# Performance work log

Hardware: AMD Instinct MI355X
Metric: run time of the kernel (lower is better)

Reference implementation:

```python
import jax, jax.numpy as jnp
import numpy as np

# dims: B=batch, CIN/COUT=channels, T=timesteps, K=kernel length (= T+1, since
# max_timesteps=2048 is even and CKConv bumps it to odd), DK=SIREN hidden width
B, CIN, COUT, T, DK = 32, 32, 32, 2048, 32
K = T + 1


def setup_inputs() -> dict:
    key = jax.random.key(0)
    ks = jax.random.split(key, 9)
    u = lambda k, shape, lim: jax.random.uniform(k, shape, minval=-lim, maxval=lim)
    # SIREN layer 1 (Conv1d 1->DK, k=1): first layer init uniform(-1, 1)
    w1 = u(ks[0], (DK, 1), 1.0)
    b1 = u(ks[1], (DK,), 1.0)          # torch bias init: U(-1/sqrt(fan_in)), fan_in=1
    # SIREN layer 2 (DK->DK): uniform(-sqrt(6/DK)/omega0, +), omega0=1
    siren_val = float(np.sqrt(6.0 / DK))
    w2 = u(ks[2], (DK, DK), siren_val)
    b2 = u(ks[3], (DK,), float(1.0 / np.sqrt(DK)))
    # output layer (DK -> CIN*COUT)
    w3 = u(ks[4], (CIN * COUT, DK), siren_val)
    b3 = u(ks[5], (CIN * COUT,), float(1.0 / np.sqrt(DK)))
    omega1 = jnp.asarray(1.0, jnp.float32)
    omega2 = jnp.asarray(1.0, jnp.float32)
    bias = jax.random.normal(ks[6], (COUT,), jnp.float32)   # CKConv output bias
    x = jax.random.normal(ks[7], (B, CIN, T), jnp.float32)
    rel_pos = jnp.linspace(-1.0, 1.0, K, dtype=jnp.float32)  # buffer _rel_positions
    return dict(x=x, rel_pos=rel_pos, w1=w1, b1=b1, omega1=omega1,
                w2=w2, b2=b2, omega2=omega2, w3=w3, b3=b3, bias=bias)


def reference(x, rel_pos, w1, b1, omega1, w2, b2, omega2, w3, b3, bias):
    # --- SIREN kernel network: 1x1 convs over the K positions == matmuls ---
    pos = rel_pos[None, :]                                   # (1, K)
    h = jnp.sin(omega1 * (w1 @ pos + b1[:, None]))           # (DK, K)
    h = jnp.sin(omega2 * (w2 @ h + b2[:, None]))             # (DK, K)
    kern = (w3 @ h + b3[:, None]).reshape(COUT, CIN, K)      # (COUT, CIN, K)
    # --- causal conv: left-pad by K-1 zeros, then valid cross-correlation ---
    out = jax.lax.conv_general_dilated(
        x, kern, window_strides=(1,), padding=[(K - 1, 0)],
        dimension_numbers=("NCH", "OIH", "NCH"))             # (B, COUT, T)
    return out + bias[None, :, None]
```

## Files before the change

### kernel.cpp

```cpp
#include <hip/hip_runtime.h>
#include <hip/hip_bf16.h>
#include <stdint.h>

typedef short bf16x8 __attribute__((ext_vector_type(8)));
typedef float f32x16 __attribute__((ext_vector_type(16)));

#define T 2048
#define KLEN 2049
#define DK 32
#define NCO 32
#define NCI 32
#define NB 32

#define GR 2216
#define SREF 2055
#define WT_CH 257
#define WT_ELEMS (NCI*WT_CH*NCO*8)
#define XR_ELEMS (NB*NCI*GR)

#define WT_OFF 0
#define XR_OFF (WT_ELEMS*2)
#define XRS_OFF (XR_OFF + XR_ELEMS*2)

#define CIB 528
#define GPC 1056
#define GPCP 1088
#define CPYB 17472
#define BUFB (2*CPYB)
#define LDS_TOT (2*BUFB)

__global__ __launch_bounds__(256) void gen_w(
    const float* __restrict__ rel_pos,
    const float* __restrict__ w1, const float* __restrict__ b1, const float* __restrict__ om1,
    const float* __restrict__ w2, const float* __restrict__ b2, const float* __restrict__ om2,
    const float* __restrict__ w3, const float* __restrict__ b3,
    uint16_t* __restrict__ Wt)
{
    __shared__ float h1s[8][32];
    __shared__ float h2s[8][32];
    int t = threadIdx.x;
    int dchunk = blockIdx.x;
    int dd = t >> 5, i = t & 31;
    int d = (dchunk << 3) + dd;
    float pos = (d < KLEN) ? rel_pos[2048 - d] : 0.f;
    h1s[dd][i] = sinf(om1[0] * (w1[i] * pos + b1[i]));
    __syncthreads();
    {
        float a = b2[i];
        #pragma unroll
        for (int j = 0; j < 32; ++j) a += w2[i*32 + j] * h1s[dd][j];
        h2s[dd][i] = sinf(om2[0] * a);
    }
    __syncthreads();
    for (int r = 0; r < 4; ++r) {
        int tt = t + (r << 8);
        int ci = tt >> 5, co = tt & 31;
        int coci = (co << 5) + ci;
        float w3r[32];
        #pragma unroll
        for (int j = 0; j < 8; ++j)
            *(float4*)&w3r[j*4] = *(const float4*)&w3[coci*32 + j*4];
        float bb = b3[coci];
        union { uint16_t u[8]; uint4 q; } pack;
        #pragma unroll
        for (int ddd = 0; ddd < 8; ++ddd) {
            float a = bb;
            #pragma unroll
            for (int j = 0; j < 32; ++j) a += w3r[j] * h2s[ddd][j];
            if (((dchunk << 3) + ddd) >= KLEN) a = 0.f;
            __hip_bfloat16 hv = __float2bfloat16(a);
            pack.u[ddd] = *(uint16_t*)&hv;
        }
        *(uint4*)&Wt[((ci*WT_CH + dchunk)*NCO + co) << 3] = pack.q;
    }
}

__global__ __launch_bounds__(256) void gen_x(const float* __restrict__ x,
                                             uint16_t* __restrict__ xr,
                                             uint16_t* __restrict__ xrs)
{
    int idx = blockIdx.x*256 + threadIdx.x;
    if (idx >= NB*NCI*GR) return;
    int row = idx / GR;
    int g = idx - row*GR;
    int s = SREF - g;
    float v  = (s  >= 0 && s  < T) ? x[row*T + s]  : 0.f;
    int s2 = s - 1;
    float v2 = (s2 >= 0 && s2 < T) ? x[row*T + s2] : 0.f;
    __hip_bfloat16 hv = __float2bfloat16(v);
    __hip_bfloat16 hv2 = __float2bfloat16(v2);
    xr[idx]  = *(uint16_t*)&hv;
    xrs[idx] = *(uint16_t*)&hv2;
}

__device__ __forceinline__ void gld16(const uint16_t* g, char* l)
{
    typedef const __attribute__((address_space(1))) uint32_t GU;
    typedef __attribute__((address_space(3))) uint32_t LU;
    __builtin_amdgcn_global_load_lds((GU*)g, (LU*)l, 16, 0, 0);
}

__global__ __launch_bounds__(512, 4) void conv(
    const uint16_t* __restrict__ Wt, const uint16_t* __restrict__ xr,
    const float* __restrict__ bias, float* __restrict__ out)
{
    __shared__ uint4 lds4[LDS_TOT/16];
    char* ldsb = (char*)lds4;
    float* red = (float*)lds4;
    int tid = threadIdx.x;
    int b = blockIdx.x & 31;
    int q = blockIdx.x >> 5;
    int p = q & 7;
    int th = (q < 8) ? (63 - (p << 2)) : ((p << 2) + 3);
    int nw = (th + 1) >> 2;
    int g0base = 2016 - (th << 5);
    int w = tid >> 6, lane = tid & 63, n = lane & 31, hi = lane >> 5;
    int cig = w;

    int srcE[5], dstC[5];
    #pragma unroll
    for (int k = 0; k < 5; ++k) {
        int gi = tid + (k << 9);
        if (gi < 2176) {
            int cpy = gi >= GPCP;
            int j = gi - cpy*GPCP;
            dstC[k] = cpy*CPYB + (j << 4);
            if (j < GPC) {
                int ci = (j*1986) >> 16;
                int qq = j - ci*33;
                srcE[k] = (cpy ? XR_ELEMS : 0) + (b*NCI + ci)*GR + (qq << 3);
            } else srcE[k] = 0;
        } else { srcE[k] = 0; dstC[k] = -1; }
    }

    int obase = 39 - n + (hi << 3);
    int par = obase & 1;
    int bbb = cig*CIB + par*CPYB + ((obase - par) << 1);

    f32x16 acc0, acc1, acc2, acc3;
    #pragma unroll
    for (int r = 0; r < 16; ++r) { acc0[r]=0.f; acc1[r]=0.f; acc2[r]=0.f; acc3[r]=0.f; }

    #define STAGE(BUF, GOFF) { \
        _Pragma("unroll") \
        for (int k = 0; k < 5; ++k) \
            if (dstC[k] >= 0) gld16(xr + srcE[k] + (GOFF), (BUF) + dstC[k]); }

    STAGE(ldsb, g0base)
    __syncthreads();

    for (int wi = 0; wi < nw; ++wi) {
        int cur = wi & 1;
        if (wi + 1 < nw) {
            char* bufn = ldsb + (cur ^ 1)*BUFB;
            int g0n = g0base + ((wi + 1) << 7);
            STAGE(bufn, g0n)
        }
        int dcw = wi << 4;
        const char* rbase = ldsb + cur*BUFB + bbb;

        #pragma unroll
        for (int cii = 0; cii < 4; ++cii) {
            int ci = (cii << 3) + cig;
            const uint16_t* aB = Wt + (((ci*WT_CH + dcw + hi)*NCO + n) << 3);
            bf16x8 av0 = *(const bf16x8*)(aB);
            bf16x8 av1 = *(const bf16x8*)(aB + 512);
            bf16x8 av2 = *(const bf16x8*)(aB + 1024);
            bf16x8 av3 = *(const bf16x8*)(aB + 1536);
            bf16x8 av4 = *(const bf16x8*)(aB + 2048);
            bf16x8 av5 = *(const bf16x8*)(aB + 2560);
            bf16x8 av6 = *(const bf16x8*)(aB + 3072);
            bf16x8 av7 = *(const bf16x8*)(aB + 3584);
            const char* pbase = rbase + cii*(8*CIB);

            #define RDBB(MM) union { uint32_t u_[4]; bf16x8 v; } bb; { \
                const char* pp = pbase + ((MM) << 5); \
                bb.u_[0] = *(const uint32_t*)(pp); \
                bb.u_[1] = *(const uint32_t*)(pp + 4); \
                bb.u_[2] = *(const uint32_t*)(pp + 8); \
                bb.u_[3] = *(const uint32_t*)(pp + 12); }
            #define MF(AC, AV) AC = __builtin_amdgcn_mfma_f32_32x32x16_bf16(AV, bb.v, AC, 0,0,0);

            { RDBB(0)  MF(acc0, av0) }
            { RDBB(1)  MF(acc0, av1) }
            { RDBB(2)  MF(acc0, av2) MF(acc1, av0) }
            { RDBB(3)  MF(acc0, av3) MF(acc1, av1) }
            { RDBB(4)  MF(acc0, av4) MF(acc1, av2) MF(acc2, av0) }
            { RDBB(5)  MF(acc0, av5) MF(acc1, av3) MF(acc2, av1) }
            { RDBB(6)  MF(acc0, av6) MF(acc1, av4) MF(acc2, av2) MF(acc3, av0) }
            { RDBB(7)  MF(acc0, av7) MF(acc1, av5) MF(acc2, av3) MF(acc3, av1) }
            { RDBB(8)  MF(acc1, av6) MF(acc2, av4) MF(acc3, av2) }
            { RDBB(9)  MF(acc1, av7) MF(acc2, av5) MF(acc3, av3) }
            { RDBB(10) MF(acc2, av6) MF(acc3, av4) }
            { RDBB(11) MF(acc2, av7) MF(acc3, av5) }
            { RDBB(12) MF(acc3, av6) }
            { RDBB(13) MF(acc3, av7) }
            #undef MF
            #undef RDBB
        }
        __syncthreads();
    }
    #undef STAGE

    #pragma unroll
    for (int dlt = 0; dlt < 4; ++dlt) {
        f32x16 a = (dlt == 0) ? acc0 : (dlt == 1) ? acc1 : (dlt == 2) ? acc2 : acc3;
        __syncthreads();
        if (w < 4) {
            #pragma unroll
            for (int r = 0; r < 16; ++r)
                red[(w*16 + r)*64 + lane] = a[r];
        }
        __syncthreads();
        if (w >= 4) {
            #pragma unroll
            for (int r = 0; r < 16; ++r)
                red[((w-4)*16 + r)*64 + lane] += a[r];
        }
        __syncthreads();
        int t0 = (th - dlt) << 5;
        #pragma unroll
        for (int h = 0; h < 2; ++h) {
            int e = tid + (h << 9);
            int lane_e = e & 63;
            int reg = e >> 6;
            float s = 0.f;
            #pragma unroll
            for (int ww = 0; ww < 4; ++ww) s += red[(ww*16 + reg)*64 + lane_e];
            int co = (reg & 3) + ((reg >> 2) << 3) + ((lane_e >> 5) << 2);
            int t = t0 + (lane_e & 31);
            out[(b*NCO + co)*T + t] = s + bias[co];
        }
    }
}

extern "C" void kernel_launch(void* const* d_in, const int* in_sizes, int n_in,
                              void* d_out, int out_size, void* d_ws, size_t ws_size,
                              hipStream_t stream)
{
    const float* x       = (const float*)d_in[0];
    const float* rel_pos = (const float*)d_in[1];
    const float* w1  = (const float*)d_in[2];
    const float* b1  = (const float*)d_in[3];
    const float* om1 = (const float*)d_in[4];
    const float* w2  = (const float*)d_in[5];
    const float* b2  = (const float*)d_in[6];
    const float* om2 = (const float*)d_in[7];
    const float* w3  = (const float*)d_in[8];
    const float* b3  = (const float*)d_in[9];
    const float* bias = (const float*)d_in[10];
    float* out = (float*)d_out;
    char* ws = (char*)d_ws;
    uint16_t* Wt  = (uint16_t*)(ws + WT_OFF);
    uint16_t* xrp = (uint16_t*)(ws + XR_OFF);
    uint16_t* xrs = (uint16_t*)(ws + XRS_OFF);

    hipLaunchKernelGGL(gen_w, dim3(WT_CH), dim3(256), 0, stream,
                       rel_pos, w1, b1, om1, w2, b2, om2, w3, b3, Wt);
    int n2 = NB*NCI*GR;
    hipLaunchKernelGGL(gen_x, dim3((n2+255)/256), dim3(256), 0, stream, x, xrp, xrs);
    hipLaunchKernelGGL(conv, dim3(NB*16), dim3(512), 0, stream, Wt, xrp, bias, out);
}
```

Before: 151.4 us.

## Merge weight and input prep kernels, double-buffer B fragments, raise MFMA priority

Combines the SIREN weight-generation and input-reversal kernels into one launch, with block ranges dispatched by blockIdx, which removes one kernel launch and lets both kinds of work run concurrently. In the conv inner loop, B-fragment LDS reads switch from four 32-bit loads to two 64-bit loads. Those reads are software-pipelined into two alternating registers so each load is issued one step ahead of the MFMAs that use it. The MFMA section is wrapped in s_setprio(1)/s_setprio(0) to favour issuing math wavefronts. GENX_BLOCKS uses floor division, which is exact here because NB*NCI*GR is divisible by 256.

```diff
diff --git a/kernel.cpp b/kernel.cpp
--- a/kernel.cpp
+++ b/kernel.cpp
@@ -4,6 +4,7 @@
 
 typedef short bf16x8 __attribute__((ext_vector_type(8)));
 typedef float f32x16 __attribute__((ext_vector_type(16)));
+typedef uint32_t u32x2 __attribute__((ext_vector_type(2), aligned(4)));
 
 #define T 2048
 #define KLEN 2049
@@ -29,68 +30,68 @@
 #define BUFB (2*CPYB)
 #define LDS_TOT (2*BUFB)
 
-__global__ __launch_bounds__(256) void gen_w(
+#define GENX_BLOCKS ((NB*NCI*GR)/256)
+
+__global__ __launch_bounds__(256) void gen(
     const float* __restrict__ rel_pos,
     const float* __restrict__ w1, const float* __restrict__ b1, const float* __restrict__ om1,
     const float* __restrict__ w2, const float* __restrict__ b2, const float* __restrict__ om2,
     const float* __restrict__ w3, const float* __restrict__ b3,
-    uint16_t* __restrict__ Wt)
+    const float* __restrict__ x,
+    uint16_t* __restrict__ Wt, uint16_t* __restrict__ xr, uint16_t* __restrict__ xrs)
 {
     __shared__ float h1s[8][32];
     __shared__ float h2s[8][32];
     int t = threadIdx.x;
-    int dchunk = blockIdx.x;
-    int dd = t >> 5, i = t & 31;
-    int d = (dchunk << 3) + dd;
-    float pos = (d < KLEN) ? rel_pos[2048 - d] : 0.f;
-    h1s[dd][i] = sinf(om1[0] * (w1[i] * pos + b1[i]));
-    __syncthreads();
-    {
-        float a = b2[i];
-        #pragma unroll
-        for (int j = 0; j < 32; ++j) a += w2[i*32 + j] * h1s[dd][j];
-        h2s[dd][i] = sinf(om2[0] * a);
-    }
-    __syncthreads();
-    for (int r = 0; r < 4; ++r) {
-        int tt = t + (r << 8);
-        int ci = tt >> 5, co = tt & 31;
-        int coci = (co << 5) + ci;
-        float w3r[32];
-        #pragma unroll
-        for (int j = 0; j < 8; ++j)
-            *(float4*)&w3r[j*4] = *(const float4*)&w3[coci*32 + j*4];
-        float bb = b3[coci];
-        union { uint16_t u[8]; uint4 q; } pack;
-        #pragma unroll
-        for (int ddd = 0; ddd < 8; ++ddd) {
-            float a = bb;
-            #pragma unroll
-            for (int j = 0; j < 32; ++j) a += w3r[j] * h2s[ddd][j];
-            if (((dchunk << 3) + ddd) >= KLEN) a = 0.f;
-            __hip_bfloat16 hv = __float2bfloat16(a);
-            pack.u[ddd] = *(uint16_t*)&hv;
-        }
-        *(uint4*)&Wt[((ci*WT_CH + dchunk)*NCO + co) << 3] = pack.q;
-    }
-}
-
-__global__ __launch_bounds__(256) void gen_x(const float* __restrict__ x,
-                                             uint16_t* __restrict__ xr,
-                                             uint16_t* __restrict__ xrs)
-{
-    int idx = blockIdx.x*256 + threadIdx.x;
-    if (idx >= NB*NCI*GR) return;
-    int row = idx / GR;
-    int g = idx - row*GR;
-    int s = SREF - g;
-    float v  = (s  >= 0 && s  < T) ? x[row*T + s]  : 0.f;
-    int s2 = s - 1;
-    float v2 = (s2 >= 0 && s2 < T) ? x[row*T + s2] : 0.f;
-    __hip_bfloat16 hv = __float2bfloat16(v);
-    __hip_bfloat16 hv2 = __float2bfloat16(v2);
-    xr[idx]  = *(uint16_t*)&hv;
-    xrs[idx] = *(uint16_t*)&hv2;
+    if (blockIdx.x < WT_CH) {
+        int dchunk = blockIdx.x;
+        int dd = t >> 5, i = t & 31;
+        int d = (dchunk << 3) + dd;
+        float pos = (d < KLEN) ? rel_pos[2048 - d] : 0.f;
+        h1s[dd][i] = sinf(om1[0] * (w1[i] * pos + b1[i]));
+        __syncthreads();
+        {
+            float a = b2[i];
+            #pragma unroll
+            for (int j = 0; j < 32; ++j) a += w2[i*32 + j] * h1s[dd][j];
+            h2s[dd][i] = sinf(om2[0] * a);
+        }
+        __syncthreads();
+        for (int r = 0; r < 4; ++r) {
+            int tt = t + (r << 8);
+            int ci = tt >> 5, co = tt & 31;
+            int coci = (co << 5) + ci;
+            float w3r[32];
+            #pragma unroll
+            for (int j = 0; j < 8; ++j)
+                *(float4*)&w3r[j*4] = *(const float4*)&w3[coci*32 + j*4];
+            float bb = b3[coci];
+            union { uint16_t u[8]; uint4 qv; } pack;
+            #pragma unroll
+            for (int ddd = 0; ddd < 8; ++ddd) {
+                float a = bb;
+                #pragma unroll
+                for (int j = 0; j < 32; ++j) a += w3r[j] * h2s[ddd][j];
+                if (((dchunk << 3) + ddd) >= KLEN) a = 0.f;
+                __hip_bfloat16 hv = __float2bfloat16(a);
+                pack.u[ddd] = *(uint16_t*)&hv;
+            }
+            *(uint4*)&Wt[((ci*WT_CH + dchunk)*NCO + co) << 3] = pack.qv;
+        }
+    } else {
+        int idx = (blockIdx.x - WT_CH)*256 + t;
+        if (idx >= NB*NCI*GR) return;
+        int row = idx / GR;
+        int g = idx - row*GR;
+        int s = SREF - g;
+        float v  = (s  >= 0 && s  < T) ? x[row*T + s]  : 0.f;
+        int s2 = s - 1;
+        float v2 = (s2 >= 0 && s2 < T) ? x[row*T + s2] : 0.f;
+        __hip_bfloat16 hv = __float2bfloat16(v);
+        __hip_bfloat16 hv2 = __float2bfloat16(v2);
+        xr[idx]  = *(uint16_t*)&hv;
+        xrs[idx] = *(uint16_t*)&hv2;
+    }
 }
 
 __device__ __forceinline__ void gld16(const uint16_t* g, char* l)
@@ -159,6 +160,7 @@
         int dcw = wi << 4;
         const char* rbase = ldsb + cur*BUFB + bbb;
 
+        __builtin_amdgcn_s_setprio(1);
         #pragma unroll
         for (int cii = 0; cii < 4; ++cii) {
             int ci = (cii << 3) + cig;
@@ -173,31 +175,33 @@
             bf16x8 av7 = *(const bf16x8*)(aB + 3584);
             const char* pbase = rbase + cii*(8*CIB);
 
-            #define RDBB(MM) union { uint32_t u_[4]; bf16x8 v; } bb; { \
+            #define LOADF(DST, MM) { \
                 const char* pp = pbase + ((MM) << 5); \
-                bb.u_[0] = *(const uint32_t*)(pp); \
-                bb.u_[1] = *(const uint32_t*)(pp + 4); \
-                bb.u_[2] = *(const uint32_t*)(pp + 8); \
-                bb.u_[3] = *(const uint32_t*)(pp + 12); }
-            #define MF(AC, AV) AC = __builtin_amdgcn_mfma_f32_32x32x16_bf16(AV, bb.v, AC, 0,0,0);
-
-            { RDBB(0)  MF(acc0, av0) }
-            { RDBB(1)  MF(acc0, av1) }
-            { RDBB(2)  MF(acc0, av2) MF(acc1, av0) }
-            { RDBB(3)  MF(acc0, av3) MF(acc1, av1) }
-            { RDBB(4)  MF(acc0, av4) MF(acc1, av2) MF(acc2, av0) }
-            { RDBB(5)  MF(acc0, av5) MF(acc1, av3) MF(acc2, av1) }
-            { RDBB(6)  MF(acc0, av6) MF(acc1, av4) MF(acc2, av2) MF(acc3, av0) }
-            { RDBB(7)  MF(acc0, av7) MF(acc1, av5) MF(acc2, av3) MF(acc3, av1) }
-            { RDBB(8)  MF(acc1, av6) MF(acc2, av4) MF(acc3, av2) }
-            { RDBB(9)  MF(acc1, av7) MF(acc2, av5) MF(acc3, av3) }
-            { RDBB(10) MF(acc2, av6) MF(acc3, av4) }
-            { RDBB(11) MF(acc2, av7) MF(acc3, av5) }
-            { RDBB(12) MF(acc3, av6) }
-            { RDBB(13) MF(acc3, av7) }
+                (DST).d[0] = *(const u32x2*)(pp); \
+                (DST).d[1] = *(const u32x2*)(pp + 8); }
+            #define MF(AC, AV, BV) AC = __builtin_amdgcn_mfma_f32_32x32x16_bf16(AV, BV, AC, 0,0,0);
+
+            union FB { u32x2 d[2]; bf16x8 v; } f0, f1;
+            LOADF(f0, 0)
+            LOADF(f1, 1)
+            MF(acc0, av0, f0.v)                                          LOADF(f0, 2)
+            MF(acc0, av1, f1.v)                                          LOADF(f1, 3)
+            MF(acc0, av2, f0.v) MF(acc1, av0, f0.v)                      LOADF(f0, 4)
+            MF(acc0, av3, f1.v) MF(acc1, av1, f1.v)                      LOADF(f1, 5)
+            MF(acc0, av4, f0.v) MF(acc1, av2, f0.v) MF(acc2, av0, f0.v)  LOADF(f0, 6)
+            MF(acc0, av5, f1.v) MF(acc1, av3, f1.v) MF(acc2, av1, f1.v)  LOADF(f1, 7)
+            MF(acc0, av6, f0.v) MF(acc1, av4, f0.v) MF(acc2, av2, f0.v) MF(acc3, av0, f0.v) LOADF(f0, 8)
+            MF(acc0, av7, f1.v) MF(acc1, av5, f1.v) MF(acc2, av3, f1.v) MF(acc3, av1, f1.v) LOADF(f1, 9)
+            MF(acc1, av6, f0.v) MF(acc2, av4, f0.v) MF(acc3, av2, f0.v)  LOADF(f0, 10)
+            MF(acc1, av7, f1.v) MF(acc2, av5, f1.v) MF(acc3, av3, f1.v)  LOADF(f1, 11)
+            MF(acc2, av6, f0.v) MF(acc3, av4, f0.v)                      LOADF(f0, 12)
+            MF(acc2, av7, f1.v) MF(acc3, av5, f1.v)                      LOADF(f1, 13)
+            MF(acc3, av6, f0.v)
+            MF(acc3, av7, f1.v)
             #undef MF
-            #undef RDBB
-        }
+            #undef LOADF
+        }
+        __builtin_amdgcn_s_setprio(0);
         __syncthreads();
     }
     #undef STAGE
@@ -255,9 +259,7 @@
     uint16_t* xrp = (uint16_t*)(ws + XR_OFF);
     uint16_t* xrs = (uint16_t*)(ws + XRS_OFF);
 
-    hipLaunchKernelGGL(gen_w, dim3(WT_CH), dim3(256), 0, stream,
-                       rel_pos, w1, b1, om1, w2, b2, om2, w3, b3, Wt);
-    int n2 = NB*NCI*GR;
-    hipLaunchKernelGGL(gen_x, dim3((n2+255)/256), dim3(256), 0, stream, x, xrp, xrs);
+    hipLaunchKernelGGL(gen, dim3(WT_CH + GENX_BLOCKS), dim3(256), 0, stream,
+                       rel_pos, w1, b1, om1, w2, b2, om2, w3, b3, x, Wt, xrp, xrs);
     hipLaunchKernelGGL(conv, dim3(NB*16), dim3(512), 0, stream, Wt, xrp, bias, out);
 }
```

Result: slower. 161.4 us (+6.6%).
